# Performance work log

Hardware: AMD Instinct MI355X
Metric: run time of the kernel (lower is better)

## Reference

```python
import jax, jax.numpy as jnp
import numpy as np

N_QUBITS = 4
BATCH = 65536
D_IN = 512


def _rx(theta):
    # PennyLane RX(theta) = [[cos(t/2), -i sin(t/2)], [-i sin(t/2), cos(t/2)]]
    c = jnp.cos(theta / 2).astype(jnp.complex64)
    s = jnp.sin(theta / 2).astype(jnp.complex64)
    return jnp.stack([jnp.stack([c, -1j * s]), jnp.stack([-1j * s, c])])


def _rot(phi, theta, omega):
    # PennyLane Rot = RZ(omega) RY(theta) RZ(phi)
    c = jnp.cos(theta / 2).astype(jnp.complex64)
    s = jnp.sin(theta / 2).astype(jnp.complex64)
    em = jnp.exp(-0.5j * (phi + omega).astype(jnp.complex64))
    ep = jnp.exp(0.5j * (phi + omega).astype(jnp.complex64))
    emd = jnp.exp(-0.5j * (phi - omega).astype(jnp.complex64))
    epd = jnp.exp(0.5j * (phi - omega).astype(jnp.complex64))
    return jnp.stack([jnp.stack([em * c, -epd * s]), jnp.stack([emd * s, ep * c])])


def _apply1(state, U, wire):
    # state: (2,)*N_QUBITS, wire 0 = most significant (PennyLane convention)
    s = jnp.tensordot(U, state, axes=((1,), (wire,)))
    return jnp.moveaxis(s, 0, wire)


def _cnot(state, ctrl, tgt):
    s = jnp.moveaxis(state, (ctrl, tgt), (0, 1))
    s = jnp.stack([s[0], s[1][::-1]], axis=0)  # flip target where ctrl==1
    return jnp.moveaxis(s, (0, 1), (ctrl, tgt))


def _circuit(angles, w):
    # angles: (4,), w: (2, 4, 3)
    state = jnp.zeros((2,) * N_QUBITS, jnp.complex64).at[(0,) * N_QUBITS].set(1.0)
    # AngleEmbedding (default rotation = X)
    for i in range(N_QUBITS):
        state = _apply1(state, _rx(angles[i]), i)
    # StronglyEntanglingLayers
    n_layers = w.shape[0]
    for l in range(n_layers):
        for i in range(N_QUBITS):
            state = _apply1(state, _rot(w[l, i, 0], w[l, i, 1], w[l, i, 2]), i)
        r = (l % (N_QUBITS - 1)) + 1  # default ranges
        for i in range(N_QUBITS):
            state = _cnot(state, i, (i + r) % N_QUBITS)
    p = jnp.abs(state) ** 2
    z = jnp.stack([p.take(0, axis=i).sum() - p.take(1, axis=i).sum()
                   for i in range(N_QUBITS)])
    return z.mean()


def setup_inputs() -> dict:
    key = jax.random.key(0)
    k1, k2, k3, k4 = jax.random.split(key, 4)
    return {
        "x": jax.random.normal(k1, (BATCH, D_IN), dtype=jnp.float32),
        "fc_w": jax.random.normal(k2, (N_QUBITS, D_IN), dtype=jnp.float32) * 0.05,
        "fc_b": jax.random.normal(k3, (N_QUBITS,), dtype=jnp.float32) * 0.05,
        "w": jax.random.normal(k4, (2, N_QUBITS, 3), dtype=jnp.float32),
    }


def reference(x, fc_w, fc_b, w):
    angles = jnp.tanh(x @ fc_w.T + fc_b)  # (B, 4)
    return jax.vmap(lambda a: _circuit(a, w))(angles)  # (B,)
```

## Files before the change

### kernel.cpp

```cpp
#include <hip/hip_runtime.h>
#include <hip/hip_bf16.h>
#include <cstddef>

#define D_IN 512
#define ROWS_PER_WAVE 8
#define ROWS_PER_BLOCK 32

__global__ __launch_bounds__(256) void qhead_gemm(
    const float* __restrict__ x,
    const float* __restrict__ fc_w,
    float* __restrict__ dots, int B)
{
    const int t    = threadIdx.x;
    const int lane = t & 63;
    const int wv   = t >> 6;
    const int sub  = lane & 31;
    const int half = lane >> 5;

    const float4* w4 = (const float4*)fc_w;
    float4 wreg[4][4];
#pragma unroll
    for (int j = 0; j < 4; ++j)
#pragma unroll
        for (int it = 0; it < 4; ++it)
            wreg[j][it] = w4[j * 128 + it * 32 + sub];

    const int row0 = blockIdx.x * ROWS_PER_BLOCK + wv * ROWS_PER_WAVE;

#pragma unroll
    for (int p = 0; p < 4; ++p) {
        const int r = row0 + p * 2 + half;
        if (r >= B) return;
        const float4* xr = (const float4*)(x + (size_t)r * D_IN);

        float4 xv[4];
#pragma unroll
        for (int it = 0; it < 4; ++it) xv[it] = xr[it * 32 + sub];

        float s0 = 0.f, s1 = 0.f, s2 = 0.f, s3 = 0.f;
#pragma unroll
        for (int it = 0; it < 4; ++it) {
            float4 v = xv[it];
            s0 += v.x * wreg[0][it].x + v.y * wreg[0][it].y
                + v.z * wreg[0][it].z + v.w * wreg[0][it].w;
            s1 += v.x * wreg[1][it].x + v.y * wreg[1][it].y
                + v.z * wreg[1][it].z + v.w * wreg[1][it].w;
            s2 += v.x * wreg[2][it].x + v.y * wreg[2][it].y
                + v.z * wreg[2][it].z + v.w * wreg[2][it].w;
            s3 += v.x * wreg[3][it].x + v.y * wreg[3][it].y
                + v.z * wreg[3][it].z + v.w * wreg[3][it].w;
        }

#pragma unroll
        for (int off = 1; off < 32; off <<= 1) {
            s0 += __shfl_xor(s0, off);
            s1 += __shfl_xor(s1, off);
            s2 += __shfl_xor(s2, off);
            s3 += __shfl_xor(s3, off);
        }

        if (sub < 4) {
            float v = (sub == 0) ? s0 : (sub == 1) ? s1 : (sub == 2) ? s2 : s3;
            dots[(size_t)r * 4 + sub] = v;
        }
    }
}

template<int BIT>
__device__ __forceinline__ void applyG(float* sr, float* si,
    float u00r, float u00i, float u01r, float u01i,
    float u10r, float u10i, float u11r, float u11i)
{
#pragma unroll
    for (int m = 0; m < 8; ++m) {
        const int lo = m & (BIT - 1);
        const int i0 = ((m ^ lo) << 1) | lo;
        const int i1 = i0 | BIT;
        float a0r = sr[i0], a0i = si[i0];
        float a1r = sr[i1], a1i = si[i1];
        float n0r = u00r * a0r - u00i * a0i + u01r * a1r - u01i * a1i;
        float n0i = u00r * a0i + u00i * a0r + u01r * a1i + u01i * a1r;
        float n1r = u10r * a0r - u10i * a0i + u11r * a1r - u11i * a1i;
        float n1i = u10r * a0i + u10i * a0r + u11r * a1i + u11i * a1r;
        sr[i0] = n0r; si[i0] = n0i;
        sr[i1] = n1r; si[i1] = n1i;
    }
}

template<int CB, int TB>
__device__ __forceinline__ void applyCNOT(float* sr, float* si)
{
    constexpr int FREE = 15 & ~CB & ~TB;
    constexpr int LO = FREE & (-FREE);
    constexpr int HI = FREE ^ LO;
#pragma unroll
    for (int m = 0; m < 4; ++m) {
        const int idx = CB | ((m & 1) ? LO : 0) | ((m & 2) ? HI : 0);
        const int j = idx | TB;
        float tr = sr[idx]; sr[idx] = sr[j]; sr[j] = tr;
        float ti = si[idx]; si[idx] = si[j]; si[j] = ti;
    }
}

__global__ __launch_bounds__(256) void qhead_sim(
    const float* __restrict__ dots,
    const float* __restrict__ fc_b,
    const float* __restrict__ w,
    float* __restrict__ out, int B)
{
    const int r = blockIdx.x * 256 + threadIdx.x;
    if (r >= B) return;

    float rm[8][8];
#pragma unroll
    for (int g = 0; g < 8; ++g) {
        float phi = w[g * 3 + 0];
        float th  = w[g * 3 + 1];
        float om  = w[g * 3 + 2];
        float sn, cs;  sincosf(th * 0.5f, &sn, &cs);
        float sa, ca;  sincosf((phi + om) * 0.5f, &sa, &ca);
        float sd, cd;  sincosf((phi - om) * 0.5f, &sd, &cd);
        rm[g][0] =  cs * ca;  rm[g][1] = -cs * sa;
        rm[g][2] = -sn * cd;  rm[g][3] = -sn * sd;
        rm[g][4] =  sn * cd;  rm[g][5] = -sn * sd;
        rm[g][6] =  cs * ca;  rm[g][7] =  cs * sa;
    }

    float4 d = ((const float4*)dots)[r];
    const float ang0 = tanhf(d.x + fc_b[0]);
    const float ang1 = tanhf(d.y + fc_b[1]);
    const float ang2 = tanhf(d.z + fc_b[2]);
    const float ang3 = tanhf(d.w + fc_b[3]);

    float sr[16], si[16];
#pragma unroll
    for (int i = 0; i < 16; ++i) { sr[i] = 0.f; si[i] = 0.f; }
    sr[0] = 1.f;

    {
        float hs, hc;
        sincosf(ang0 * 0.5f, &hs, &hc);
        applyG<8>(sr, si, hc, 0.f, 0.f, -hs, 0.f, -hs, hc, 0.f);
        sincosf(ang1 * 0.5f, &hs, &hc);
        applyG<4>(sr, si, hc, 0.f, 0.f, -hs, 0.f, -hs, hc, 0.f);
        sincosf(ang2 * 0.5f, &hs, &hc);
        applyG<2>(sr, si, hc, 0.f, 0.f, -hs, 0.f, -hs, hc, 0.f);
        sincosf(ang3 * 0.5f, &hs, &hc);
        applyG<1>(sr, si, hc, 0.f, 0.f, -hs, 0.f, -hs, hc, 0.f);
    }

#define ROTG(l, q)                                                          \
    applyG<(1 << (3 - (q)))>(sr, si,                                        \
        rm[(l) * 4 + (q)][0], rm[(l) * 4 + (q)][1], rm[(l) * 4 + (q)][2],   \
        rm[(l) * 4 + (q)][3], rm[(l) * 4 + (q)][4], rm[(l) * 4 + (q)][5],   \
        rm[(l) * 4 + (q)][6], rm[(l) * 4 + (q)][7]);

    ROTG(0, 0); ROTG(0, 1); ROTG(0, 2); ROTG(0, 3);
    applyCNOT<8, 4>(sr, si);
    applyCNOT<4, 2>(sr, si);
    applyCNOT<2, 1>(sr, si);
    applyCNOT<1, 8>(sr, si);

    ROTG(1, 0); ROTG(1, 1); ROTG(1, 2); ROTG(1, 3);
    applyCNOT<8, 2>(sr, si);
    applyCNOT<4, 1>(sr, si);
    applyCNOT<2, 8>(sr, si);
    applyCNOT<1, 4>(sr, si);
#undef ROTG

    float res = 0.f;
#pragma unroll
    for (int i = 0; i < 16; ++i) {
        float p = sr[i] * sr[i] + si[i] * si[i];
        res += p * (1.0f - 0.5f * (float)__popc(i));
    }
    out[r] = res;
}

extern "C" void kernel_launch(void* const* d_in, const int* in_sizes, int n_in,
                              void* d_out, int out_size, void* d_ws, size_t ws_size,
                              hipStream_t stream)
{
    const float* x    = (const float*)d_in[0];
    const float* fc_w = (const float*)d_in[1];
    const float* fc_b = (const float*)d_in[2];
    const float* w    = (const float*)d_in[3];
    float* out  = (float*)d_out;
    float* dots = (float*)d_ws;

    const int B = in_sizes[0] / D_IN;

    qhead_gemm<<<(B + ROWS_PER_BLOCK - 1) / ROWS_PER_BLOCK, 256, 0, stream>>>(
        x, fc_w, dots, B);
    qhead_sim<<<(B + 255) / 256, 256, 0, stream>>>(dots, fc_b, w, out, B);
}
```

Measured before the change: 34.08 us.

## Precompute circuit observable as 16x16 quadratic form and fuse with GEMM

```diff
diff --git a/kernel.cpp b/kernel.cpp
--- a/kernel.cpp
+++ b/kernel.cpp
@@ -3,68 +3,8 @@
 #include <cstddef>
 
 #define D_IN 512
-#define ROWS_PER_WAVE 8
-#define ROWS_PER_BLOCK 32
-
-__global__ __launch_bounds__(256) void qhead_gemm(
-    const float* __restrict__ x,
-    const float* __restrict__ fc_w,
-    float* __restrict__ dots, int B)
-{
-    const int t    = threadIdx.x;
-    const int lane = t & 63;
-    const int wv   = t >> 6;
-    const int sub  = lane & 31;
-    const int half = lane >> 5;
-
-    const float4* w4 = (const float4*)fc_w;
-    float4 wreg[4][4];
-#pragma unroll
-    for (int j = 0; j < 4; ++j)
-#pragma unroll
-        for (int it = 0; it < 4; ++it)
-            wreg[j][it] = w4[j * 128 + it * 32 + sub];
-
-    const int row0 = blockIdx.x * ROWS_PER_BLOCK + wv * ROWS_PER_WAVE;
-
-#pragma unroll
-    for (int p = 0; p < 4; ++p) {
-        const int r = row0 + p * 2 + half;
-        if (r >= B) return;
-        const float4* xr = (const float4*)(x + (size_t)r * D_IN);
-
-        float4 xv[4];
-#pragma unroll
-        for (int it = 0; it < 4; ++it) xv[it] = xr[it * 32 + sub];
-
-        float s0 = 0.f, s1 = 0.f, s2 = 0.f, s3 = 0.f;
-#pragma unroll
-        for (int it = 0; it < 4; ++it) {
-            float4 v = xv[it];
-            s0 += v.x * wreg[0][it].x + v.y * wreg[0][it].y
-                + v.z * wreg[0][it].z + v.w * wreg[0][it].w;
-            s1 += v.x * wreg[1][it].x + v.y * wreg[1][it].y
-                + v.z * wreg[1][it].z + v.w * wreg[1][it].w;
-            s2 += v.x * wreg[2][it].x + v.y * wreg[2][it].y
-                + v.z * wreg[2][it].z + v.w * wreg[2][it].w;
-            s3 += v.x * wreg[3][it].x + v.y * wreg[3][it].y
-                + v.z * wreg[3][it].z + v.w * wreg[3][it].w;
-        }
-
-#pragma unroll
-        for (int off = 1; off < 32; off <<= 1) {
-            s0 += __shfl_xor(s0, off);
-            s1 += __shfl_xor(s1, off);
-            s2 += __shfl_xor(s2, off);
-            s3 += __shfl_xor(s3, off);
-        }
-
-        if (sub < 4) {
-            float v = (sub == 0) ? s0 : (sub == 1) ? s1 : (sub == 2) ? s2 : s3;
-            dots[(size_t)r * 4 + sub] = v;
-        }
-    }
-}
+#define BLOCK 256
+#define RPB 32
 
 template<int BIT>
 __device__ __forceinline__ void applyG(float* sr, float* si,
@@ -102,14 +42,10 @@
     }
 }
 
-__global__ __launch_bounds__(256) void qhead_sim(
-    const float* __restrict__ dots,
-    const float* __restrict__ fc_b,
-    const float* __restrict__ w,
-    float* __restrict__ out, int B)
-{
-    const int r = blockIdx.x * 256 + threadIdx.x;
-    if (r >= B) return;
+__global__ void qhead_pre(const float* __restrict__ w, float* __restrict__ M)
+{
+    __shared__ float VR[16][16], VI[16][16];
+    const int j = threadIdx.x;
 
     float rm[8][8];
 #pragma unroll
@@ -126,28 +62,11 @@
         rm[g][6] =  cs * ca;  rm[g][7] =  cs * sa;
     }
 
-    float4 d = ((const float4*)dots)[r];
-    const float ang0 = tanhf(d.x + fc_b[0]);
-    const float ang1 = tanhf(d.y + fc_b[1]);
-    const float ang2 = tanhf(d.z + fc_b[2]);
-    const float ang3 = tanhf(d.w + fc_b[3]);
-
-    float sr[16], si[16];
-#pragma unroll
-    for (int i = 0; i < 16; ++i) { sr[i] = 0.f; si[i] = 0.f; }
-    sr[0] = 1.f;
-
-    {
-        float hs, hc;
-        sincosf(ang0 * 0.5f, &hs, &hc);
-        applyG<8>(sr, si, hc, 0.f, 0.f, -hs, 0.f, -hs, hc, 0.f);
-        sincosf(ang1 * 0.5f, &hs, &hc);
-        applyG<4>(sr, si, hc, 0.f, 0.f, -hs, 0.f, -hs, hc, 0.f);
-        sincosf(ang2 * 0.5f, &hs, &hc);
-        applyG<2>(sr, si, hc, 0.f, 0.f, -hs, 0.f, -hs, hc, 0.f);
-        sincosf(ang3 * 0.5f, &hs, &hc);
-        applyG<1>(sr, si, hc, 0.f, 0.f, -hs, 0.f, -hs, hc, 0.f);
-    }
+    if (j < 16) {
+        float sr[16], si[16];
+#pragma unroll
+        for (int i = 0; i < 16; ++i) { sr[i] = 0.f; si[i] = 0.f; }
+        sr[j] = 1.f;
 
 #define ROTG(l, q)                                                          \
     applyG<(1 << (3 - (q)))>(sr, si,                                        \
@@ -155,26 +74,162 @@
         rm[(l) * 4 + (q)][3], rm[(l) * 4 + (q)][4], rm[(l) * 4 + (q)][5],   \
         rm[(l) * 4 + (q)][6], rm[(l) * 4 + (q)][7]);
 
-    ROTG(0, 0); ROTG(0, 1); ROTG(0, 2); ROTG(0, 3);
-    applyCNOT<8, 4>(sr, si);
-    applyCNOT<4, 2>(sr, si);
-    applyCNOT<2, 1>(sr, si);
-    applyCNOT<1, 8>(sr, si);
-
-    ROTG(1, 0); ROTG(1, 1); ROTG(1, 2); ROTG(1, 3);
-    applyCNOT<8, 2>(sr, si);
-    applyCNOT<4, 1>(sr, si);
-    applyCNOT<2, 8>(sr, si);
-    applyCNOT<1, 4>(sr, si);
+        ROTG(0, 0); ROTG(0, 1); ROTG(0, 2); ROTG(0, 3);
+        applyCNOT<8, 4>(sr, si);
+        applyCNOT<4, 2>(sr, si);
+        applyCNOT<2, 1>(sr, si);
+        applyCNOT<1, 8>(sr, si);
+        ROTG(1, 0); ROTG(1, 1); ROTG(1, 2); ROTG(1, 3);
+        applyCNOT<8, 2>(sr, si);
+        applyCNOT<4, 1>(sr, si);
+        applyCNOT<2, 8>(sr, si);
+        applyCNOT<1, 4>(sr, si);
 #undef ROTG
 
-    float res = 0.f;
-#pragma unroll
-    for (int i = 0; i < 16; ++i) {
-        float p = sr[i] * sr[i] + si[i] * si[i];
-        res += p * (1.0f - 0.5f * (float)__popc(i));
-    }
-    out[r] = res;
+        const int pm = __popc(j) & 3;
+#pragma unroll
+        for (int k = 0; k < 16; ++k) {
+            float re = sr[k], im = si[k], vr, vi;
+            if      (pm == 0) { vr =  re; vi =  im; }
+            else if (pm == 1) { vr =  im; vi = -re; }
+            else if (pm == 2) { vr = -re; vi = -im; }
+            else              { vr = -im; vi =  re; }
+            VR[k][j] = vr;  VI[k][j] = vi;
+        }
+    }
+    __syncthreads();
+    if (j < 16) {
+#pragma unroll
+        for (int b = 0; b < 16; ++b) {
+            float acc = 0.f;
+#pragma unroll
+            for (int k = 0; k < 16; ++k) {
+                float wk = 1.0f - 0.5f * (float)__popc(k);
+                acc += wk * (VR[k][j] * VR[k][b] + VI[k][j] * VI[k][b]);
+            }
+            M[j * 16 + b] = acc;
+        }
+    }
+}
+
+__global__ __launch_bounds__(BLOCK) void qhead_main(
+    const float* __restrict__ x,
+    const float* __restrict__ fc_w,
+    const float* __restrict__ fc_b,
+    const float* __restrict__ Mg,
+    float* __restrict__ out, int B)
+{
+    __shared__ float part[RPB][4][36];
+    __shared__ float ang[RPB][4];
+    __shared__ float Mlds[256];
+
+    const int t    = threadIdx.x;
+    Mlds[t] = Mg[t];
+
+    const int lane = t & 63;
+    const int wv   = t >> 6;
+    const int sub  = lane & 31;
+    const int half = lane >> 5;
+    const int row0 = blockIdx.x * RPB + wv * 8;
+
+    const float4* w4 = (const float4*)fc_w;
+    float4 wreg[4][4];
+#pragma unroll
+    for (int jj = 0; jj < 4; ++jj)
+#pragma unroll
+        for (int it = 0; it < 4; ++it)
+            wreg[jj][it] = w4[jj * 128 + it * 32 + sub];
+
+    int rp0 = row0 + 0 + half; if (rp0 >= B) rp0 = B - 1;
+    int rp1 = row0 + 2 + half; if (rp1 >= B) rp1 = B - 1;
+    int rp2 = row0 + 4 + half; if (rp2 >= B) rp2 = B - 1;
+    int rp3 = row0 + 6 + half; if (rp3 >= B) rp3 = B - 1;
+    const float4* x4 = (const float4*)x;
+
+#define LOADX(dst, r)                                                       \
+    {                                                                       \
+        const float4* xr = x4 + (size_t)(r) * 128 + sub;                    \
+        dst[0] = xr[0]; dst[1] = xr[32]; dst[2] = xr[64]; dst[3] = xr[96];  \
+    }
+#define PASS(p, xv)                                                         \
+    {                                                                       \
+        float s0 = 0.f, s1 = 0.f, s2 = 0.f, s3 = 0.f;                       \
+        _Pragma("unroll")                                                   \
+        for (int it = 0; it < 4; ++it) {                                    \
+            float4 v = xv[it];                                              \
+            s0 += v.x * wreg[0][it].x + v.y * wreg[0][it].y                 \
+                + v.z * wreg[0][it].z + v.w * wreg[0][it].w;                \
+            s1 += v.x * wreg[1][it].x + v.y * wreg[1][it].y                 \
+                + v.z * wreg[1][it].z + v.w * wreg[1][it].w;                \
+            s2 += v.x * wreg[2][it].x + v.y * wreg[2][it].y                 \
+                + v.z * wreg[2][it].z + v.w * wreg[2][it].w;                \
+            s3 += v.x * wreg[3][it].x + v.y * wreg[3][it].y                 \
+                + v.z * wreg[3][it].z + v.w * wreg[3][it].w;                \
+        }                                                                   \
+        const int lr = wv * 8 + (p) * 2 + half;                             \
+        part[lr][0][sub] = s0;  part[lr][1][sub] = s1;                      \
+        part[lr][2][sub] = s2;  part[lr][3][sub] = s3;                      \
+    }
+
+    float4 xvA[4], xvB[4];
+    LOADX(xvA, rp0);
+    LOADX(xvB, rp1);
+    PASS(0, xvA);
+    LOADX(xvA, rp2);
+    PASS(1, xvB);
+    LOADX(xvB, rp3);
+    PASS(2, xvA);
+    PASS(3, xvB);
+#undef LOADX
+#undef PASS
+
+    __syncthreads();
+
+    if (t < 128) {
+        const int row = t >> 2, jj = t & 3;
+        const float4* pv = (const float4*)&part[row][jj][0];
+        float4 a = pv[0];
+#pragma unroll
+        for (int u = 1; u < 8; ++u) {
+            float4 b = pv[u];
+            a.x += b.x; a.y += b.y; a.z += b.z; a.w += b.w;
+        }
+        float s = (a.x + a.y) + (a.z + a.w);
+        ang[row][jj] = tanhf(s + fc_b[jj]);
+    }
+    __syncthreads();
+
+    if (t < 32) {
+        const int grow = blockIdx.x * RPB + t;
+        float c[4], s[4];
+#pragma unroll
+        for (int q = 0; q < 4; ++q)
+            sincosf(ang[t][q] * 0.5f, &s[q], &c[q]);
+
+        float rA[4] = { c[0]*c[1], c[0]*s[1], s[0]*c[1], s[0]*s[1] };
+        float rB[4] = { c[2]*c[3], c[2]*s[3], s[2]*c[3], s[2]*s[3] };
+        float r[16];
+#pragma unroll
+        for (int u = 0; u < 4; ++u)
+#pragma unroll
+            for (int v = 0; v < 4; ++v)
+                r[u * 4 + v] = rA[u] * rB[v];
+
+        const float4* M4 = (const float4*)Mlds;
+        float res = 0.f;
+#pragma unroll
+        for (int a = 0; a < 16; ++a) {
+            float ta = 0.f;
+#pragma unroll
+            for (int bq = 0; bq < 4; ++bq) {
+                float4 m = M4[a * 4 + bq];
+                ta += m.x * r[bq * 4 + 0] + m.y * r[bq * 4 + 1]
+                    + m.z * r[bq * 4 + 2] + m.w * r[bq * 4 + 3];
+            }
+            res += ta * r[a];
+        }
+        if (grow < B) out[grow] = res;
+    }
 }
 
 extern "C" void kernel_launch(void* const* d_in, const int* in_sizes, int n_in,
@@ -185,12 +240,12 @@
     const float* fc_w = (const float*)d_in[1];
     const float* fc_b = (const float*)d_in[2];
     const float* w    = (const float*)d_in[3];
-    float* out  = (float*)d_out;
-    float* dots = (float*)d_ws;
+    float* out = (float*)d_out;
+    float* M   = (float*)d_ws;
 
     const int B = in_sizes[0] / D_IN;
 
-    qhead_gemm<<<(B + ROWS_PER_BLOCK - 1) / ROWS_PER_BLOCK, 256, 0, stream>>>(
-        x, fc_w, dots, B);
-    qhead_sim<<<(B + 255) / 256, 256, 0, stream>>>(dots, fc_b, w, out, B);
-}
+    qhead_pre<<<1, 64, 0, stream>>>(w, M);
+    qhead_main<<<(B + RPB - 1) / RPB, BLOCK, 0, stream>>>(
+        x, fc_w, fc_b, M, out, B);
+}
```

New measurement: 44.46 us. +30.5%, slower.

## Fuse GEMM and circuit sim via precomputed 16x16 observable quadratic form

Applied to the files above, without the earlier changes.

```diff
diff --git a/kernel.cpp b/kernel.cpp
--- a/kernel.cpp
+++ b/kernel.cpp
@@ -3,68 +3,12 @@
 #include <cstddef>
 
 #define D_IN 512
-#define ROWS_PER_WAVE 8
-#define ROWS_PER_BLOCK 32
-
-__global__ __launch_bounds__(256) void qhead_gemm(
-    const float* __restrict__ x,
-    const float* __restrict__ fc_w,
-    float* __restrict__ dots, int B)
-{
-    const int t    = threadIdx.x;
-    const int lane = t & 63;
-    const int wv   = t >> 6;
-    const int sub  = lane & 31;
-    const int half = lane >> 5;
-
-    const float4* w4 = (const float4*)fc_w;
-    float4 wreg[4][4];
-#pragma unroll
-    for (int j = 0; j < 4; ++j)
-#pragma unroll
-        for (int it = 0; it < 4; ++it)
-            wreg[j][it] = w4[j * 128 + it * 32 + sub];
-
-    const int row0 = blockIdx.x * ROWS_PER_BLOCK + wv * ROWS_PER_WAVE;
-
-#pragma unroll
-    for (int p = 0; p < 4; ++p) {
-        const int r = row0 + p * 2 + half;
-        if (r >= B) return;
-        const float4* xr = (const float4*)(x + (size_t)r * D_IN);
-
-        float4 xv[4];
-#pragma unroll
-        for (int it = 0; it < 4; ++it) xv[it] = xr[it * 32 + sub];
-
-        float s0 = 0.f, s1 = 0.f, s2 = 0.f, s3 = 0.f;
-#pragma unroll
-        for (int it = 0; it < 4; ++it) {
-            float4 v = xv[it];
-            s0 += v.x * wreg[0][it].x + v.y * wreg[0][it].y
-                + v.z * wreg[0][it].z + v.w * wreg[0][it].w;
-            s1 += v.x * wreg[1][it].x + v.y * wreg[1][it].y
-                + v.z * wreg[1][it].z + v.w * wreg[1][it].w;
-            s2 += v.x * wreg[2][it].x + v.y * wreg[2][it].y
-                + v.z * wreg[2][it].z + v.w * wreg[2][it].w;
-            s3 += v.x * wreg[3][it].x + v.y * wreg[3][it].y
-                + v.z * wreg[3][it].z + v.w * wreg[3][it].w;
-        }
-
-#pragma unroll
-        for (int off = 1; off < 32; off <<= 1) {
-            s0 += __shfl_xor(s0, off);
-            s1 += __shfl_xor(s1, off);
-            s2 += __shfl_xor(s2, off);
-            s3 += __shfl_xor(s3, off);
-        }
-
-        if (sub < 4) {
-            float v = (sub == 0) ? s0 : (sub == 1) ? s1 : (sub == 2) ? s2 : s3;
-            dots[(size_t)r * 4 + sub] = v;
-        }
-    }
-}
+#define BLOCK 256
+#define RPB 32
+
+typedef float f4 __attribute__((ext_vector_type(4)));
+
+#define NTLOAD(p) __builtin_nontemporal_load(p)
 
 template<int BIT>
 __device__ __forceinline__ void applyG(float* sr, float* si,
@@ -102,79 +46,163 @@
     }
 }
 
-__global__ __launch_bounds__(256) void qhead_sim(
-    const float* __restrict__ dots,
+__global__ __launch_bounds__(BLOCK) void qhead_fused(
+    const float* __restrict__ x,
+    const float* __restrict__ fc_w,
     const float* __restrict__ fc_b,
     const float* __restrict__ w,
     float* __restrict__ out, int B)
 {
-    const int r = blockIdx.x * 256 + threadIdx.x;
-    if (r >= B) return;
-
-    float rm[8][8];
-#pragma unroll
-    for (int g = 0; g < 8; ++g) {
-        float phi = w[g * 3 + 0];
-        float th  = w[g * 3 + 1];
-        float om  = w[g * 3 + 2];
-        float sn, cs;  sincosf(th * 0.5f, &sn, &cs);
-        float sa, ca;  sincosf((phi + om) * 0.5f, &sa, &ca);
-        float sd, cd;  sincosf((phi - om) * 0.5f, &sd, &cd);
-        rm[g][0] =  cs * ca;  rm[g][1] = -cs * sa;
-        rm[g][2] = -sn * cd;  rm[g][3] = -sn * sd;
-        rm[g][4] =  sn * cd;  rm[g][5] = -sn * sd;
-        rm[g][6] =  cs * ca;  rm[g][7] =  cs * sa;
-    }
-
-    float4 d = ((const float4*)dots)[r];
-    const float ang0 = tanhf(d.x + fc_b[0]);
-    const float ang1 = tanhf(d.y + fc_b[1]);
-    const float ang2 = tanhf(d.z + fc_b[2]);
-    const float ang3 = tanhf(d.w + fc_b[3]);
-
-    float sr[16], si[16];
-#pragma unroll
-    for (int i = 0; i < 16; ++i) { sr[i] = 0.f; si[i] = 0.f; }
-    sr[0] = 1.f;
-
-    {
-        float hs, hc;
-        sincosf(ang0 * 0.5f, &hs, &hc);
-        applyG<8>(sr, si, hc, 0.f, 0.f, -hs, 0.f, -hs, hc, 0.f);
-        sincosf(ang1 * 0.5f, &hs, &hc);
-        applyG<4>(sr, si, hc, 0.f, 0.f, -hs, 0.f, -hs, hc, 0.f);
-        sincosf(ang2 * 0.5f, &hs, &hc);
-        applyG<2>(sr, si, hc, 0.f, 0.f, -hs, 0.f, -hs, hc, 0.f);
-        sincosf(ang3 * 0.5f, &hs, &hc);
-        applyG<1>(sr, si, hc, 0.f, 0.f, -hs, 0.f, -hs, hc, 0.f);
-    }
-
-#define ROTG(l, q)                                                          \
-    applyG<(1 << (3 - (q)))>(sr, si,                                        \
-        rm[(l) * 4 + (q)][0], rm[(l) * 4 + (q)][1], rm[(l) * 4 + (q)][2],   \
-        rm[(l) * 4 + (q)][3], rm[(l) * 4 + (q)][4], rm[(l) * 4 + (q)][5],   \
-        rm[(l) * 4 + (q)][6], rm[(l) * 4 + (q)][7]);
-
-    ROTG(0, 0); ROTG(0, 1); ROTG(0, 2); ROTG(0, 3);
-    applyCNOT<8, 4>(sr, si);
-    applyCNOT<4, 2>(sr, si);
-    applyCNOT<2, 1>(sr, si);
-    applyCNOT<1, 8>(sr, si);
-
-    ROTG(1, 0); ROTG(1, 1); ROTG(1, 2); ROTG(1, 3);
-    applyCNOT<8, 2>(sr, si);
-    applyCNOT<4, 1>(sr, si);
-    applyCNOT<2, 8>(sr, si);
-    applyCNOT<1, 4>(sr, si);
+    __shared__ float VR[16][16], VI[16][16];
+    __shared__ float Mlds[256];
+
+    const int t    = threadIdx.x;
+    const int lane = t & 63;
+    const int wv   = t >> 6;
+    const int sub  = lane & 31;
+    const int half = lane >> 5;
+    const int row0w = blockIdx.x * RPB + wv * 8;
+
+    if (wv == 0) {
+        float sr[16], si[16];
+#pragma unroll
+        for (int i = 0; i < 16; ++i) {
+            sr[i] = (i == lane) ? 1.f : 0.f;
+            si[i] = 0.f;
+        }
+
+#define ROTG(g, q)                                                          \
+        {                                                                   \
+            float phi = w[(g) * 3 + 0], th = w[(g) * 3 + 1],                \
+                  om  = w[(g) * 3 + 2];                                     \
+            float sn, cs;  sincosf(th * 0.5f, &sn, &cs);                    \
+            float sa, ca;  sincosf((phi + om) * 0.5f, &sa, &ca);            \
+            float sd, cd;  sincosf((phi - om) * 0.5f, &sd, &cd);            \
+            applyG<(1 << (3 - (q)))>(sr, si,  cs * ca, -cs * sa,            \
+                                     -sn * cd, -sn * sd,                    \
+                                      sn * cd, -sn * sd,                    \
+                                      cs * ca,  cs * sa);                   \
+        }
+        ROTG(0, 0) ROTG(1, 1) ROTG(2, 2) ROTG(3, 3)
+        applyCNOT<8, 4>(sr, si);
+        applyCNOT<4, 2>(sr, si);
+        applyCNOT<2, 1>(sr, si);
+        applyCNOT<1, 8>(sr, si);
+        ROTG(4, 0) ROTG(5, 1) ROTG(6, 2) ROTG(7, 3)
+        applyCNOT<8, 2>(sr, si);
+        applyCNOT<4, 1>(sr, si);
+        applyCNOT<2, 8>(sr, si);
+        applyCNOT<1, 4>(sr, si);
 #undef ROTG
 
-    float res = 0.f;
-#pragma unroll
-    for (int i = 0; i < 16; ++i) {
-        float p = sr[i] * sr[i] + si[i] * si[i];
-        res += p * (1.0f - 0.5f * (float)__popc(i));
-    }
-    out[r] = res;
+        if (lane < 16) {
+            const int pm = __popc(lane) & 3;
+#pragma unroll
+            for (int k = 0; k < 16; ++k) {
+                float re = sr[k], im = si[k];
+                float vr = (pm == 0) ? re : (pm == 1) ? im
+                         : (pm == 2) ? -re : -im;
+                float vi = (pm == 0) ? im : (pm == 1) ? -re
+                         : (pm == 2) ? -im : re;
+                VR[k][lane] = vr;  VI[k][lane] = vi;
+            }
+        }
+#pragma unroll
+        for (int q = 0; q < 4; ++q) {
+            const int e = lane + q * 64;
+            const int j = e >> 4, b = e & 15;
+            float acc = 0.f;
+#pragma unroll
+            for (int k = 0; k < 16; ++k) {
+                const float wk = 1.0f - 0.5f * (float)__popc(k);
+                acc += wk * (VR[k][j] * VR[k][b] + VI[k][j] * VI[k][b]);
+            }
+            Mlds[e] = acc;
+        }
+    }
+
+    const f4* w4 = (const f4*)fc_w;
+    f4 wreg[4][4];
+#pragma unroll
+    for (int jj = 0; jj < 4; ++jj)
+#pragma unroll
+        for (int it = 0; it < 4; ++it)
+            wreg[jj][it] = w4[jj * 128 + it * 32 + sub];
+
+    const f4* x4 = (const f4*)x;
+    float kd0 = 0.f, kd1 = 0.f, kd2 = 0.f, kd3 = 0.f;
+
+#pragma unroll
+    for (int p = 0; p < 4; ++p) {
+        int rp = row0w + p * 2 + half;
+        if (rp >= B) rp = B - 1;
+        const f4* xr = x4 + (size_t)rp * 128 + sub;
+
+        f4 v0 = NTLOAD(xr);
+        f4 v1 = NTLOAD(xr + 32);
+        f4 v2 = NTLOAD(xr + 64);
+        f4 v3 = NTLOAD(xr + 96);
+
+        float s0 = 0.f, s1 = 0.f, s2 = 0.f, s3 = 0.f;
+#pragma unroll
+        for (int c = 0; c < 4; ++c) {
+            f4 v = (c == 0) ? v0 : (c == 1) ? v1 : (c == 2) ? v2 : v3;
+            s0 += v[0]*wreg[0][c][0] + v[1]*wreg[0][c][1]
+                + v[2]*wreg[0][c][2] + v[3]*wreg[0][c][3];
+            s1 += v[0]*wreg[1][c][0] + v[1]*wreg[1][c][1]
+                + v[2]*wreg[1][c][2] + v[3]*wreg[1][c][3];
+            s2 += v[0]*wreg[2][c][0] + v[1]*wreg[2][c][1]
+                + v[2]*wreg[2][c][2] + v[3]*wreg[2][c][3];
+            s3 += v[0]*wreg[3][c][0] + v[1]*wreg[3][c][1]
+                + v[2]*wreg[3][c][2] + v[3]*wreg[3][c][3];
+        }
+
+#pragma unroll
+        for (int off = 1; off < 32; off <<= 1) {
+            s0 += __shfl_xor(s0, off);
+            s1 += __shfl_xor(s1, off);
+            s2 += __shfl_xor(s2, off);
+            s3 += __shfl_xor(s3, off);
+        }
+
+        if (sub == p) { kd0 = s0; kd1 = s1; kd2 = s2; kd3 = s3; }
+    }
+
+    __syncthreads();
+
+    if (sub < 4) {
+        const int row = row0w + sub * 2 + half;
+
+        float c0, c1, c2, c3, s0, s1, s2, s3;
+        sincosf(tanhf(kd0 + fc_b[0]) * 0.5f, &s0, &c0);
+        sincosf(tanhf(kd1 + fc_b[1]) * 0.5f, &s1, &c1);
+        sincosf(tanhf(kd2 + fc_b[2]) * 0.5f, &s2, &c2);
+        sincosf(tanhf(kd3 + fc_b[3]) * 0.5f, &s3, &c3);
+
+        float rA[4] = { c0*c1, c0*s1, s0*c1, s0*s1 };
+        float rB[4] = { c2*c3, c2*s3, s2*c3, s2*s3 };
+        float r[16];
+#pragma unroll
+        for (int u = 0; u < 4; ++u)
+#pragma unroll
+            for (int v = 0; v < 4; ++v)
+                r[u * 4 + v] = rA[u] * rB[v];
+
+        const f4* M4 = (const f4*)Mlds;
+        float res = 0.f;
+#pragma unroll
+        for (int a = 0; a < 16; ++a) {
+            float ta = 0.f;
+#pragma unroll
+            for (int bq = 0; bq < 4; ++bq) {
+                f4 m = M4[a * 4 + bq];
+                ta += m[0] * r[bq * 4 + 0] + m[1] * r[bq * 4 + 1]
+                    + m[2] * r[bq * 4 + 2] + m[3] * r[bq * 4 + 3];
+            }
+            res += ta * r[a];
+        }
+        if (row < B) out[row] = res;
+    }
 }
 
 extern "C" void kernel_launch(void* const* d_in, const int* in_sizes, int n_in,
@@ -185,12 +213,10 @@
     const float* fc_w = (const float*)d_in[1];
     const float* fc_b = (const float*)d_in[2];
     const float* w    = (const float*)d_in[3];
-    float* out  = (float*)d_out;
-    float* dots = (float*)d_ws;
+    float* out = (float*)d_out;
 
     const int B = in_sizes[0] / D_IN;
 
-    qhead_gemm<<<(B + ROWS_PER_BLOCK - 1) / ROWS_PER_BLOCK, 256, 0, stream>>>(
-        x, fc_w, dots, B);
-    qhead_sim<<<(B + 255) / 256, 256, 0, stream>>>(dots, fc_b, w, out, B);
-}
+    qhead_fused<<<(B + RPB - 1) / RPB, BLOCK, 0, stream>>>(
+        x, fc_w, fc_b, w, out, B);
+}
```

After: 56.39 us. 1.65x slower.
